# Kernel tuning notes

Measured on AMD Instinct MI355X. Metric: run time of the kernel, lower is better.

The kernel has to match this reference:

```python
import jax, jax.numpy as jnp
import numpy as np

B, N, D, NS, H, ITERS = 64, 4096, 64, 7, 128, 3
EPS = 1e-8
SCALE = D ** -0.5
LN_EPS = 1e-5


def layernorm(x, g, b):
    m = x.mean(-1, keepdims=True)
    v = ((x - m) ** 2).mean(-1, keepdims=True)
    return (x - m) / jnp.sqrt(v + LN_EPS) * g + b


def gru_cell(x, h, W_ih, W_hh, b_ih, b_hh):
    # torch.nn.GRUCell semantics
    gi = x @ W_ih.T + b_ih
    gh = h @ W_hh.T + b_hh
    i_r, i_z, i_n = jnp.split(gi, 3, axis=-1)
    h_r, h_z, h_n = jnp.split(gh, 3, axis=-1)
    r = jax.nn.sigmoid(i_r + h_r)
    z = jax.nn.sigmoid(i_z + h_z)
    n = jnp.tanh(i_n + r * h_n)
    return (1.0 - z) * n + z * h


def setup_inputs() -> dict:
    key = jax.random.key(0)
    ks = jax.random.split(key, 16)
    s = 0.02
    inp = {}
    inp['inputs'] = jax.random.normal(ks[0], (B, N, D), jnp.float32)
    inp['positional_embeddings'] = jax.random.normal(ks[1], (B, N, 4), jnp.float32)
    inp['slots_noise'] = jax.random.normal(ks[2], (B, NS, D), jnp.float32)
    inp['slots_mu'] = jax.random.normal(ks[3], (1, 1, D), jnp.float32)
    inp['slots_sigma'] = jax.random.uniform(ks[4], (1, 1, D), jnp.float32)
    inp['Wq'] = jax.random.normal(ks[5], (D, D), jnp.float32) * s
    inp['bq'] = jnp.zeros((D,), jnp.float32)
    inp['Wk'] = jax.random.normal(ks[6], (D, D), jnp.float32) * s
    inp['bk'] = jnp.zeros((D,), jnp.float32)
    inp['Wv'] = jax.random.normal(ks[7], (D, D), jnp.float32) * s
    inp['bv'] = jnp.zeros((D,), jnp.float32)
    inp['W_ih'] = jax.random.normal(ks[8], (3 * D, D), jnp.float32) * s
    inp['W_hh'] = jax.random.normal(ks[9], (3 * D, D), jnp.float32) * s
    inp['b_ih'] = jnp.zeros((3 * D,), jnp.float32)
    inp['b_hh'] = jnp.zeros((3 * D,), jnp.float32)
    inp['W1'] = jax.random.normal(ks[10], (H, D), jnp.float32) * s
    inp['b1'] = jnp.zeros((H,), jnp.float32)
    inp['W2'] = jax.random.normal(ks[11], (D, H), jnp.float32) * s
    inp['b2'] = jnp.zeros((D,), jnp.float32)
    inp['g_in'] = jnp.ones((D,), jnp.float32)
    inp['be_in'] = jnp.zeros((D,), jnp.float32)
    inp['g_sl'] = jnp.ones((D,), jnp.float32)
    inp['be_sl'] = jnp.zeros((D,), jnp.float32)
    inp['g_ff'] = jnp.ones((D,), jnp.float32)
    inp['be_ff'] = jnp.zeros((D,), jnp.float32)
    return inp


def reference(inputs, positional_embeddings, slots_noise, slots_mu, slots_sigma,
              Wq, bq, Wk, bk, Wv, bv, W_ih, W_hh, b_ih, b_hh,
              W1, b1, W2, b2, g_in, be_in, g_sl, be_sl, g_ff, be_ff):
    b, n, d = inputs.shape
    # slots ~ Normal(mu, sigma), reparameterized with externalized noise
    slots = slots_mu + slots_sigma * slots_noise  # [b, NS, d]
    x = layernorm(inputs, g_in, be_in)
    k = x @ Wk.T + bk  # [b, n, d]
    v = x @ Wv.T + bv  # [b, n, d]
    for _ in range(ITERS):
        slots_prev = slots
        s = layernorm(slots, g_sl, be_sl)
        q = s @ Wq.T + bq  # [b, NS, d]
        dots = jnp.einsum('bid,bjd->bij', q, k) * SCALE  # [b, NS, n]
        attn = jax.nn.softmax(dots, axis=1) + EPS  # softmax over slot axis
        attn = attn / attn.sum(-1, keepdims=True)  # renormalize over inputs
        updates = jnp.einsum('bjd,bij->bid', v, attn)  # [b, NS, d]
        slots = gru_cell(updates.reshape(-1, d), slots_prev.reshape(-1, d),
                         W_ih, W_hh, b_ih, b_hh).reshape(b, -1, d)
        ff = layernorm(slots, g_ff, be_ff)
        slots = slots + (jax.nn.relu(ff @ W1.T + b1) @ W2.T + b2)
    return slots
```

## Files before the change

kernel.cpp:

```cpp
#include <hip/hip_runtime.h>
#include <stdint.h>

#define BB 64
#define NN 4096
#define DD 64
#define NSL 7
#define HH 128
#define NITER 3

typedef __attribute__((ext_vector_type(8))) short short8;
typedef __attribute__((ext_vector_type(4))) float f32x4;

__device__ __forceinline__ unsigned short f2bf(float f){
    union { float f; unsigned int i; } x; x.f = f;
    unsigned int u = x.i;
    u += 0x7fffu + ((u >> 16) & 1u);
    return (unsigned short)(u >> 16);
}
__device__ __forceinline__ unsigned int pack2(float a, float b){
    return (unsigned int)f2bf(a) | ((unsigned int)f2bf(b) << 16);
}
__device__ __forceinline__ short8 f2bf8(float4 a, float4 b){
    short8 r;
    r[0]=(short)f2bf(a.x); r[1]=(short)f2bf(a.y); r[2]=(short)f2bf(a.z); r[3]=(short)f2bf(a.w);
    r[4]=(short)f2bf(b.x); r[5]=(short)f2bf(b.y); r[6]=(short)f2bf(b.z); r[7]=(short)f2bf(b.w);
    return r;
}
__device__ __forceinline__ f32x4 mfma16(short8 a, short8 b, f32x4 c){
    return __builtin_amdgcn_mfma_f32_16x16x32_bf16(a, b, c, 0, 0, 0);
}
__device__ __forceinline__ float sigm(float x){ return 1.f / (1.f + __expf(-x)); }

__global__ __launch_bounds__(256) void ln_kv_kernel(
    const float* __restrict__ inp,
    const float* __restrict__ g_in, const float* __restrict__ be_in,
    const float* __restrict__ Wk, const float* __restrict__ bk,
    const float* __restrict__ Wv, const float* __restrict__ bv,
    unsigned short* __restrict__ k_out, unsigned short* __restrict__ vT_out)
{
    __shared__ __align__(16) unsigned short xn[64 * 72];
    __shared__ __align__(16) unsigned short vt[64 * 72];
    const int t = threadIdx.x;
    const long R0 = (long)blockIdx.x * 64;

    {
        const int m = t >> 2, p = t & 3;
        const float4* rp = reinterpret_cast<const float4*>(inp + (R0 + m) * 64 + p * 16);
        float x[16];
        #pragma unroll
        for (int q4 = 0; q4 < 4; ++q4){
            float4 a = rp[q4];
            x[q4*4+0]=a.x; x[q4*4+1]=a.y; x[q4*4+2]=a.z; x[q4*4+3]=a.w;
        }
        float s = 0.f, ss = 0.f;
        #pragma unroll
        for (int e = 0; e < 16; ++e){ s += x[e]; ss += x[e]*x[e]; }
        s += __shfl_xor(s, 1); ss += __shfl_xor(ss, 1);
        s += __shfl_xor(s, 2); ss += __shfl_xor(ss, 2);
        const float mean = s * 0.015625f;
        const float var  = ss * 0.015625f - mean * mean;
        const float rstd = rsqrtf(var + 1e-5f);
        const float4* gp = reinterpret_cast<const float4*>(g_in + p * 16);
        const float4* bp = reinterpret_cast<const float4*>(be_in + p * 16);
        float gv[16], bev[16];
        #pragma unroll
        for (int q4 = 0; q4 < 4; ++q4){
            float4 a = gp[q4], bb = bp[q4];
            gv[q4*4+0]=a.x; gv[q4*4+1]=a.y; gv[q4*4+2]=a.z; gv[q4*4+3]=a.w;
            bev[q4*4+0]=bb.x; bev[q4*4+1]=bb.y; bev[q4*4+2]=bb.z; bev[q4*4+3]=bb.w;
        }
        unsigned int packed[8];
        #pragma unroll
        for (int e2 = 0; e2 < 8; ++e2){
            float a = (x[e2*2  ] - mean) * rstd * gv[e2*2  ] + bev[e2*2  ];
            float b = (x[e2*2+1] - mean) * rstd * gv[e2*2+1] + bev[e2*2+1];
            packed[e2] = pack2(a, b);
        }
        uint4* xp = reinterpret_cast<uint4*>(xn) + (m * 9 + p * 2);
        xp[0] = make_uint4(packed[0], packed[1], packed[2], packed[3]);
        xp[1] = make_uint4(packed[4], packed[5], packed[6], packed[7]);
    }
    __syncthreads();

    const int lane = t & 63, wave = t >> 6;
    const int n16 = lane & 15, quad = lane >> 4;

    short8 xf0 = *reinterpret_cast<const short8*>(xn + (wave*16 + n16)*72 +      quad*8);
    short8 xf1 = *reinterpret_cast<const short8*>(xn + (wave*16 + n16)*72 + 32 + quad*8);

    f32x4 acck[4];
    #pragma unroll
    for (int mt = 0; mt < 4; ++mt){
        const float* wp = Wk + (mt*16 + n16)*64 + quad*8;
        short8 a0 = f2bf8(*reinterpret_cast<const float4*>(wp),
                          *reinterpret_cast<const float4*>(wp + 4));
        short8 a1 = f2bf8(*reinterpret_cast<const float4*>(wp + 32),
                          *reinterpret_cast<const float4*>(wp + 36));
        f32x4 z = {0.f, 0.f, 0.f, 0.f};
        z = mfma16(a0, xf0, z);
        acck[mt] = mfma16(a1, xf1, z);
    }
    f32x4 accv[4];
    #pragma unroll
    for (int dt = 0; dt < 4; ++dt){
        const float* wp = Wv + (dt*16 + n16)*64 + quad*8;
        short8 b0 = f2bf8(*reinterpret_cast<const float4*>(wp),
                          *reinterpret_cast<const float4*>(wp + 4));
        short8 b1 = f2bf8(*reinterpret_cast<const float4*>(wp + 32),
                          *reinterpret_cast<const float4*>(wp + 36));
        f32x4 z = {0.f, 0.f, 0.f, 0.f};
        z = mfma16(xf0, b0, z);
        accv[dt] = mfma16(xf1, b1, z);
    }
    #pragma unroll
    for (int mt = 0; mt < 4; ++mt){
        const int m0 = mt*16 + quad*4;
        float4 bk4 = *reinterpret_cast<const float4*>(bk + m0);
        uint2 pk;
        pk.x = pack2(acck[mt][0] + bk4.x, acck[mt][1] + bk4.y);
        pk.y = pack2(acck[mt][2] + bk4.z, acck[mt][3] + bk4.w);
        *reinterpret_cast<uint2*>(xn + (wave*16 + n16)*72 + m0) = pk;
    }
    #pragma unroll
    for (int dt = 0; dt < 4; ++dt){
        const int d = dt*16 + n16;
        const float bias = bv[d];
        const int jl = wave*16 + quad*4;
        uint2 pk;
        pk.x = pack2(accv[dt][0] + bias, accv[dt][1] + bias);
        pk.y = pack2(accv[dt][2] + bias, accv[dt][3] + bias);
        *reinterpret_cast<uint2*>(vt + d*72 + jl) = pk;
    }
    __syncthreads();

    {
        const int j = t >> 2, sg = t & 3;
        const uint4* ksrc = reinterpret_cast<const uint4*>(xn + j*72 + sg*16);
        uint4* kdst = reinterpret_cast<uint4*>(k_out + (R0 + j)*64 + sg*16);
        kdst[0] = ksrc[0];
        kdst[1] = ksrc[1];
        const int bidx = (int)(R0 >> 12);
        const int jblk = (int)(R0 & 4095);
        const int d = j;
        const uint4* vsrc = reinterpret_cast<const uint4*>(vt + d*72 + sg*16);
        uint4* vdst = reinterpret_cast<uint4*>(vT_out + ((long)(bidx*64 + d))*4096 + jblk + sg*16);
        vdst[0] = vsrc[0];
        vdst[1] = vsrc[1];
    }
}

__global__ __launch_bounds__(256) void scan_kernel(
    const unsigned short* __restrict__ k_ws, const unsigned short* __restrict__ vT_ws,
    const float* __restrict__ q_ws, float* __restrict__ pu)
{
    __shared__ __align__(16) unsigned short at_all[4][16 * 40];
    __shared__ float red[4][8][80];
    const int t = threadIdx.x, lane = t & 63, wave = t >> 6;
    const int n16 = lane & 15, quad = lane >> 4;
    const int b = blockIdx.x >> 5, seg = blockIdx.x & 31;
    unsigned short* at = at_all[wave];

    for (int idx = lane; idx < 9 * 40; idx += 64){
        int rr = idx / 40, cc = idx - rr * 40;
        at[(7 + rr) * 40 + cc] = (rr == 0 && cc < 32) ? (unsigned short)0x3F80 : (unsigned short)0;
    }

    const int iq = (n16 < NSL) ? n16 : (NSL - 1);
    const float* qp = q_ws + (b*NSL + iq)*64;
    short8 qa0, qa1;
    {
        float4 a0 = *reinterpret_cast<const float4*>(qp + quad*8);
        float4 a1 = *reinterpret_cast<const float4*>(qp + quad*8 + 4);
        float4 b0 = *reinterpret_cast<const float4*>(qp + 32 + quad*8);
        float4 b1 = *reinterpret_cast<const float4*>(qp + 32 + quad*8 + 4);
        qa0 = f2bf8(make_float4(a0.x*0.125f,a0.y*0.125f,a0.z*0.125f,a0.w*0.125f),
                    make_float4(a1.x*0.125f,a1.y*0.125f,a1.z*0.125f,a1.w*0.125f));
        qa1 = f2bf8(make_float4(b0.x*0.125f,b0.y*0.125f,b0.z*0.125f,b0.w*0.125f),
                    make_float4(b1.x*0.125f,b1.y*0.125f,b1.z*0.125f,b1.w*0.125f));
    }

    const int j0 = seg*128 + wave*32;
    const long kbase = (long)b * NN * 64;
    const long vbase = (long)b * 64 * NN;

    #pragma unroll
    for (int tt = 0; tt < 2; ++tt){
        const unsigned short* kp = k_ws + kbase + (long)(j0 + tt*16 + n16)*64 + quad*8;
        short8 kb0 = *reinterpret_cast<const short8*>(kp);
        short8 kb1 = *reinterpret_cast<const short8*>(kp + 32);
        f32x4 dz = {0.f,0.f,0.f,0.f};
        dz = mfma16(qa0, kb0, dz);
        dz = mfma16(qa1, kb1, dz);
        float pm;
        if (quad == 0)      pm = fmaxf(fmaxf(dz[0], dz[1]), fmaxf(dz[2], dz[3]));
        else if (quad == 1) pm = fmaxf(fmaxf(dz[0], dz[1]), dz[2]);
        else                pm = -1e30f;
        pm = fmaxf(pm, __shfl_xor(pm, 16));
        float e0=0.f, e1=0.f, e2=0.f, e3=0.f;
        if (quad == 0){ e0=__expf(dz[0]-pm); e1=__expf(dz[1]-pm); e2=__expf(dz[2]-pm); e3=__expf(dz[3]-pm); }
        else if (quad == 1){ e0=__expf(dz[0]-pm); e1=__expf(dz[1]-pm); e2=__expf(dz[2]-pm); }
        float ps = e0 + e1 + e2 + e3;
        ps += __shfl_xor(ps, 16);
        const float inv = 1.f / ps;
        if (quad == 0){
            at[0*40 + tt*16 + n16] = f2bf(e0*inv);
            at[1*40 + tt*16 + n16] = f2bf(e1*inv);
            at[2*40 + tt*16 + n16] = f2bf(e2*inv);
            at[3*40 + tt*16 + n16] = f2bf(e3*inv);
        } else if (quad == 1){
            at[4*40 + tt*16 + n16] = f2bf(e0*inv);
            at[5*40 + tt*16 + n16] = f2bf(e1*inv);
            at[6*40 + tt*16 + n16] = f2bf(e2*inv);
        }
    }
    __syncthreads();

    short8 aa = *reinterpret_cast<const short8*>(at + n16*40 + quad*8);
    short8 ones;
    { const short ov = (n16 == 0) ? (short)0x3F80 : (short)0;
      #pragma unroll
      for (int z = 0; z < 8; ++z) ones[z] = ov; }

    f32x4 uacc[5];
    #pragma unroll
    for (int t2 = 0; t2 < 4; ++t2){
        const unsigned short* vp = vT_ws + vbase + (long)(t2*16 + n16)*NN + j0 + quad*8;
        short8 vb = *reinterpret_cast<const short8*>(vp);
        f32x4 z = {0.f,0.f,0.f,0.f};
        uacc[t2] = mfma16(aa, vb, z);
    }
    { f32x4 z = {0.f,0.f,0.f,0.f}; uacc[4] = mfma16(aa, ones, z); }

    if (quad < 2){
        #pragma unroll
        for (int r = 0; r < 4; ++r){
            const int i = quad*4 + r;
            #pragma unroll
            for (int t2 = 0; t2 < 5; ++t2)
                red[wave][i][t2*16 + n16] = uacc[t2][r];
        }
    }
    __syncthreads();
    for (int idx = t; idx < 640; idx += 256){
        const int i = idx / 80, cc = idx - i*80;
        float s = red[0][i][cc] + red[1][i][cc] + red[2][i][cc] + red[3][i][cc];
        pu[((long)(b*32 + seg)*8 + i)*80 + cc] = s;
    }
}

__device__ __forceinline__ float dot64(const float* x, const float* w){
    float acc = 0.f;
    const float4* w4 = reinterpret_cast<const float4*>(w);
    #pragma unroll
    for (int e4 = 0; e4 < 16; ++e4){
        float4 wv = w4[e4];
        acc += x[e4*4+0]*wv.x + x[e4*4+1]*wv.y + x[e4*4+2]*wv.z + x[e4*4+3]*wv.w;
    }
    return acc;
}
__device__ __forceinline__ float dot128(const float* x, const float* w){
    float acc = 0.f;
    const float4* w4 = reinterpret_cast<const float4*>(w);
    #pragma unroll
    for (int e4 = 0; e4 < 32; ++e4){
        float4 wv = w4[e4];
        acc += x[e4*4+0]*wv.x + x[e4*4+1]*wv.y + x[e4*4+2]*wv.z + x[e4*4+3]*wv.w;
    }
    return acc;
}

__global__ __launch_bounds__(256) void slot_update_kernel(
    const int mode, const int write_out,
    const float* __restrict__ pu,
    float* __restrict__ slots_ws, float* __restrict__ q_ws,
    const float* __restrict__ noise, const float* __restrict__ mu,
    const float* __restrict__ sigma,
    const float* __restrict__ W_ih, const float* __restrict__ W_hh,
    const float* __restrict__ b_ih, const float* __restrict__ b_hh,
    const float* __restrict__ W1, const float* __restrict__ b1,
    const float* __restrict__ W2, const float* __restrict__ b2,
    const float* __restrict__ g_sl, const float* __restrict__ be_sl,
    const float* __restrict__ g_ff, const float* __restrict__ be_ff,
    const float* __restrict__ Wq, const float* __restrict__ bq,
    float* __restrict__ out)
{
    __shared__ float hprev[64], updv[64], snew[64], ffb[64], h1[128], sfin[64], s2[64];
    __shared__ float redp[4][64], redp7[4][64];
    __shared__ float gi[192], gh[192];
    __shared__ float redA_s;
    const int t = threadIdx.x;
    const int b = blockIdx.x / NSL, i = blockIdx.x % NSL;
    const int lane = t & 63, wave = t >> 6;
    const long rowoff = (long)(b*NSL + i)*64;

    if (mode == 0){
        if (t < 64){
            float v = mu[t] + sigma[t] * noise[rowoff + t];
            sfin[t] = v;
            slots_ws[rowoff + t] = v;
        }
    } else {
        if (t < 64) hprev[t] = slots_ws[rowoff + t];
        {
            const int d = t & 63, g = t >> 6;
            float si = 0.f, s7 = 0.f;
            #pragma unroll
            for (int u = 0; u < 8; ++u){
                const float* base = pu + ((long)(b*32 + g*8 + u)*8)*80;
                si += base[i*80 + d];
                s7 += base[7*80 + d];
            }
            redp[g][d] = si; redp7[g][d] = s7;
        }
        if (wave == 0){
            float a = (lane < 32) ? pu[((long)(b*32 + lane)*8 + i)*80 + 64] : 0.f;
            #pragma unroll
            for (int m = 1; m < 64; m <<= 1) a += __shfl_xor(a, m);
            if (lane == 0) redA_s = a;
        }
        __syncthreads();
        if (t < 64){
            float ri = redp[0][t] + redp[1][t] + redp[2][t] + redp[3][t];
            float r7 = redp7[0][t] + redp7[1][t] + redp7[2][t] + redp7[3][t];
            updv[t] = (ri + 1e-8f * r7) / (redA_s + 4.096e-5f);
        }
        __syncthreads();
        for (int c = t; c < 384; c += 256){
            if (c < 192) gi[c] = b_ih[c] + dot64(updv, W_ih + c*64);
            else { int cc = c - 192; gh[cc] = b_hh[cc] + dot64(hprev, W_hh + cc*64); }
        }
        __syncthreads();
        if (t < 64){
            float rg = sigm(gi[t] + gh[t]);
            float zg = sigm(gi[64+t] + gh[64+t]);
            float ng = tanhf(gi[128+t] + rg * gh[128+t]);
            snew[t] = (1.f - zg) * ng + zg * hprev[t];
        }
        __syncthreads();
        {
            float x = snew[lane];
            float s = x, ss = x * x;
            #pragma unroll
            for (int m = 1; m < 64; m <<= 1){ s += __shfl_xor(s, m); ss += __shfl_xor(ss, m); }
            float mean = s * 0.015625f;
            float var  = ss * 0.015625f - mean * mean;
            float rstd = rsqrtf(var + 1e-5f);
            if (wave == 0) ffb[lane] = (x - mean) * rstd * g_ff[lane] + be_ff[lane];
        }
        __syncthreads();
        if (t < 128){
            float vv = b1[t] + dot64(ffb, W1 + t*64);
            h1[t] = vv > 0.f ? vv : 0.f;
        }
        __syncthreads();
        if (t < 64){
            float o = b2[t] + dot128(h1, W2 + t*128);
            float v = snew[t] + o;
            sfin[t] = v;
            slots_ws[rowoff + t] = v;
            if (write_out) out[rowoff + t] = v;
        }
    }
    __syncthreads();
    {
        float x = sfin[lane];
        float s = x, ss = x * x;
        #pragma unroll
        for (int m = 1; m < 64; m <<= 1){ s += __shfl_xor(s, m); ss += __shfl_xor(ss, m); }
        float mean = s * 0.015625f;
        float var  = ss * 0.015625f - mean * mean;
        float rstd = rsqrtf(var + 1e-5f);
        if (wave == 0) s2[lane] = (x - mean) * rstd * g_sl[lane] + be_sl[lane];
    }
    __syncthreads();
    if (t < 64) q_ws[rowoff + t] = bq[t] + dot64(s2, Wq + t*64);
}

extern "C" void kernel_launch(void* const* d_in, const int* in_sizes, int n_in,
                              void* d_out, int out_size, void* d_ws, size_t ws_size,
                              hipStream_t stream)
{
    const float* inp   = (const float*)d_in[0];
    const float* noise = (const float*)d_in[2];
    const float* mu    = (const float*)d_in[3];
    const float* sigma = (const float*)d_in[4];
    const float* Wq    = (const float*)d_in[5];
    const float* bq    = (const float*)d_in[6];
    const float* Wk    = (const float*)d_in[7];
    const float* bk    = (const float*)d_in[8];
    const float* Wv    = (const float*)d_in[9];
    const float* bv    = (const float*)d_in[10];
    const float* W_ih  = (const float*)d_in[11];
    const float* W_hh  = (const float*)d_in[12];
    const float* b_ih  = (const float*)d_in[13];
    const float* b_hh  = (const float*)d_in[14];
    const float* W1    = (const float*)d_in[15];
    const float* b1    = (const float*)d_in[16];
    const float* W2    = (const float*)d_in[17];
    const float* b2    = (const float*)d_in[18];
    const float* g_in  = (const float*)d_in[19];
    const float* be_in = (const float*)d_in[20];
    const float* g_sl  = (const float*)d_in[21];
    const float* be_sl = (const float*)d_in[22];
    const float* g_ff  = (const float*)d_in[23];
    const float* be_ff = (const float*)d_in[24];
    float* out = (float*)d_out;

    char* w = (char*)d_ws;
    unsigned short* k_ws  = (unsigned short*)(w);
    unsigned short* vT_ws = (unsigned short*)(w + 33554432);
    float* slots_ws       = (float*)(w + 67108864);
    float* q_ws           = (float*)(w + 67108864 + 114688);
    float* pu             = (float*)(w + 67108864 + 229376);

    ln_kv_kernel<<<4096, 256, 0, stream>>>(inp, g_in, be_in, Wk, bk, Wv, bv, k_ws, vT_ws);
    slot_update_kernel<<<448, 256, 0, stream>>>(0, 0, pu, slots_ws, q_ws, noise, mu, sigma,
        W_ih, W_hh, b_ih, b_hh, W1, b1, W2, b2, g_sl, be_sl, g_ff, be_ff, Wq, bq, out);
    for (int it = 0; it < NITER; ++it){
        scan_kernel<<<2048, 256, 0, stream>>>(k_ws, vT_ws, q_ws, pu);
        slot_update_kernel<<<448, 256, 0, stream>>>(1, (it == NITER - 1) ? 1 : 0,
            pu, slots_ws, q_ws, noise, mu, sigma,
            W_ih, W_hh, b_ih, b_hh, W1, b1, W2, b2, g_sl, be_sl, g_ff, be_ff, Wq, bq, out);
    }
}
```

Before: 293.0 us.

## Make LN+KV projection kernel persistent over tiles with register-resident weights

Each block now processes 8 row tiles and converts Wk and Wv to bf16 fragments only once, keeping them in registers. LayerNorm is computed directly in the MFMA operand layout with cross-lane shuffles, so the LDS staging buffers and both __syncthreads are removed. K and transposed V are written straight from the accumulators as 8-byte stores instead of going through LDS and coalesced 16-byte copies. The cost is fewer blocks (512), higher register pressure, and less coalesced global stores, especially for the vT writes, which spread across rows.

Result: faster. 264.9 us (-9.6%).

```diff
diff --git a/kernel.cpp b/kernel.cpp
--- a/kernel.cpp
+++ b/kernel.cpp
@@ -7,6 +7,7 @@
 #define NSL 7
 #define HH 128
 #define NITER 3
+#define TPT 8
 
 typedef __attribute__((ext_vector_type(8))) short short8;
 typedef __attribute__((ext_vector_type(4))) float f32x4;
@@ -38,114 +39,91 @@
     const float* __restrict__ Wv, const float* __restrict__ bv,
     unsigned short* __restrict__ k_out, unsigned short* __restrict__ vT_out)
 {
-    __shared__ __align__(16) unsigned short xn[64 * 72];
-    __shared__ __align__(16) unsigned short vt[64 * 72];
-    const int t = threadIdx.x;
-    const long R0 = (long)blockIdx.x * 64;
-
-    {
-        const int m = t >> 2, p = t & 3;
-        const float4* rp = reinterpret_cast<const float4*>(inp + (R0 + m) * 64 + p * 16);
-        float x[16];
-        #pragma unroll
-        for (int q4 = 0; q4 < 4; ++q4){
-            float4 a = rp[q4];
-            x[q4*4+0]=a.x; x[q4*4+1]=a.y; x[q4*4+2]=a.z; x[q4*4+3]=a.w;
-        }
-        float s = 0.f, ss = 0.f;
-        #pragma unroll
-        for (int e = 0; e < 16; ++e){ s += x[e]; ss += x[e]*x[e]; }
-        s += __shfl_xor(s, 1); ss += __shfl_xor(ss, 1);
-        s += __shfl_xor(s, 2); ss += __shfl_xor(ss, 2);
-        const float mean = s * 0.015625f;
-        const float var  = ss * 0.015625f - mean * mean;
-        const float rstd = rsqrtf(var + 1e-5f);
-        const float4* gp = reinterpret_cast<const float4*>(g_in + p * 16);
-        const float4* bp = reinterpret_cast<const float4*>(be_in + p * 16);
-        float gv[16], bev[16];
-        #pragma unroll
-        for (int q4 = 0; q4 < 4; ++q4){
-            float4 a = gp[q4], bb = bp[q4];
-            gv[q4*4+0]=a.x; gv[q4*4+1]=a.y; gv[q4*4+2]=a.z; gv[q4*4+3]=a.w;
-            bev[q4*4+0]=bb.x; bev[q4*4+1]=bb.y; bev[q4*4+2]=bb.z; bev[q4*4+3]=bb.w;
-        }
-        unsigned int packed[8];
-        #pragma unroll
-        for (int e2 = 0; e2 < 8; ++e2){
-            float a = (x[e2*2  ] - mean) * rstd * gv[e2*2  ] + bev[e2*2  ];
-            float b = (x[e2*2+1] - mean) * rstd * gv[e2*2+1] + bev[e2*2+1];
-            packed[e2] = pack2(a, b);
-        }
-        uint4* xp = reinterpret_cast<uint4*>(xn) + (m * 9 + p * 2);
-        xp[0] = make_uint4(packed[0], packed[1], packed[2], packed[3]);
-        xp[1] = make_uint4(packed[4], packed[5], packed[6], packed[7]);
-    }
-    __syncthreads();
-
-    const int lane = t & 63, wave = t >> 6;
+    const int t = threadIdx.x, lane = t & 63, wave = t >> 6;
     const int n16 = lane & 15, quad = lane >> 4;
 
-    short8 xf0 = *reinterpret_cast<const short8*>(xn + (wave*16 + n16)*72 +      quad*8);
-    short8 xf1 = *reinterpret_cast<const short8*>(xn + (wave*16 + n16)*72 + 32 + quad*8);
-
-    f32x4 acck[4];
+    const float4 gA = *reinterpret_cast<const float4*>(g_in + quad*8);
+    const float4 gB = *reinterpret_cast<const float4*>(g_in + quad*8 + 4);
+    const float4 gC = *reinterpret_cast<const float4*>(g_in + 32 + quad*8);
+    const float4 gD = *reinterpret_cast<const float4*>(g_in + 32 + quad*8 + 4);
+    const float4 eA = *reinterpret_cast<const float4*>(be_in + quad*8);
+    const float4 eB = *reinterpret_cast<const float4*>(be_in + quad*8 + 4);
+    const float4 eC = *reinterpret_cast<const float4*>(be_in + 32 + quad*8);
+    const float4 eD = *reinterpret_cast<const float4*>(be_in + 32 + quad*8 + 4);
+
+    short8 wka0[4], wka1[4], wvb0[4], wvb1[4];
+    float4 bk4[4];
+    float  bvs[4];
     #pragma unroll
     for (int mt = 0; mt < 4; ++mt){
         const float* wp = Wk + (mt*16 + n16)*64 + quad*8;
-        short8 a0 = f2bf8(*reinterpret_cast<const float4*>(wp),
-                          *reinterpret_cast<const float4*>(wp + 4));
-        short8 a1 = f2bf8(*reinterpret_cast<const float4*>(wp + 32),
-                          *reinterpret_cast<const float4*>(wp + 36));
-        f32x4 z = {0.f, 0.f, 0.f, 0.f};
-        z = mfma16(a0, xf0, z);
-        acck[mt] = mfma16(a1, xf1, z);
-    }
-    f32x4 accv[4];
-    #pragma unroll
-    for (int dt = 0; dt < 4; ++dt){
-        const float* wp = Wv + (dt*16 + n16)*64 + quad*8;
-        short8 b0 = f2bf8(*reinterpret_cast<const float4*>(wp),
-                          *reinterpret_cast<const float4*>(wp + 4));
-        short8 b1 = f2bf8(*reinterpret_cast<const float4*>(wp + 32),
-                          *reinterpret_cast<const float4*>(wp + 36));
-        f32x4 z = {0.f, 0.f, 0.f, 0.f};
-        z = mfma16(xf0, b0, z);
-        accv[dt] = mfma16(xf1, b1, z);
-    }
-    #pragma unroll
-    for (int mt = 0; mt < 4; ++mt){
-        const int m0 = mt*16 + quad*4;
-        float4 bk4 = *reinterpret_cast<const float4*>(bk + m0);
-        uint2 pk;
-        pk.x = pack2(acck[mt][0] + bk4.x, acck[mt][1] + bk4.y);
-        pk.y = pack2(acck[mt][2] + bk4.z, acck[mt][3] + bk4.w);
-        *reinterpret_cast<uint2*>(xn + (wave*16 + n16)*72 + m0) = pk;
-    }
-    #pragma unroll
-    for (int dt = 0; dt < 4; ++dt){
-        const int d = dt*16 + n16;
-        const float bias = bv[d];
-        const int jl = wave*16 + quad*4;
-        uint2 pk;
-        pk.x = pack2(accv[dt][0] + bias, accv[dt][1] + bias);
-        pk.y = pack2(accv[dt][2] + bias, accv[dt][3] + bias);
-        *reinterpret_cast<uint2*>(vt + d*72 + jl) = pk;
-    }
-    __syncthreads();
-
-    {
-        const int j = t >> 2, sg = t & 3;
-        const uint4* ksrc = reinterpret_cast<const uint4*>(xn + j*72 + sg*16);
-        uint4* kdst = reinterpret_cast<uint4*>(k_out + (R0 + j)*64 + sg*16);
-        kdst[0] = ksrc[0];
-        kdst[1] = ksrc[1];
-        const int bidx = (int)(R0 >> 12);
-        const int jblk = (int)(R0 & 4095);
-        const int d = j;
-        const uint4* vsrc = reinterpret_cast<const uint4*>(vt + d*72 + sg*16);
-        uint4* vdst = reinterpret_cast<uint4*>(vT_out + ((long)(bidx*64 + d))*4096 + jblk + sg*16);
-        vdst[0] = vsrc[0];
-        vdst[1] = vsrc[1];
+        wka0[mt] = f2bf8(*reinterpret_cast<const float4*>(wp),
+                         *reinterpret_cast<const float4*>(wp + 4));
+        wka1[mt] = f2bf8(*reinterpret_cast<const float4*>(wp + 32),
+                         *reinterpret_cast<const float4*>(wp + 36));
+        const float* vp = Wv + (mt*16 + n16)*64 + quad*8;
+        wvb0[mt] = f2bf8(*reinterpret_cast<const float4*>(vp),
+                         *reinterpret_cast<const float4*>(vp + 4));
+        wvb1[mt] = f2bf8(*reinterpret_cast<const float4*>(vp + 32),
+                         *reinterpret_cast<const float4*>(vp + 36));
+        bk4[mt] = *reinterpret_cast<const float4*>(bk + mt*16 + quad*4);
+        bvs[mt] = bv[mt*16 + n16];
+    }
+
+    for (int c = 0; c < TPT; ++c){
+        const long T0 = ((long)blockIdx.x * TPT + c) * 64;
+        const float* rp = inp + (T0 + wave*16 + n16) * 64;
+        float4 xa = *reinterpret_cast<const float4*>(rp + quad*8);
+        float4 xb = *reinterpret_cast<const float4*>(rp + quad*8 + 4);
+        float4 xc = *reinterpret_cast<const float4*>(rp + 32 + quad*8);
+        float4 xd = *reinterpret_cast<const float4*>(rp + 32 + quad*8 + 4);
+
+        float s  = (xa.x+xa.y+xa.z+xa.w) + (xb.x+xb.y+xb.z+xb.w)
+                 + (xc.x+xc.y+xc.z+xc.w) + (xd.x+xd.y+xd.z+xd.w);
+        float ss = (xa.x*xa.x+xa.y*xa.y+xa.z*xa.z+xa.w*xa.w)
+                 + (xb.x*xb.x+xb.y*xb.y+xb.z*xb.z+xb.w*xb.w)
+                 + (xc.x*xc.x+xc.y*xc.y+xc.z*xc.z+xc.w*xc.w)
+                 + (xd.x*xd.x+xd.y*xd.y+xd.z*xd.z+xd.w*xd.w);
+        s  += __shfl_xor(s, 16);  ss += __shfl_xor(ss, 16);
+        s  += __shfl_xor(s, 32);  ss += __shfl_xor(ss, 32);
+        const float mean = s * 0.015625f;
+        const float rstd = rsqrtf(ss * 0.015625f - mean*mean + 1e-5f);
+
+        float4 ya, yb, yc, yd;
+        ya.x=(xa.x-mean)*rstd*gA.x+eA.x; ya.y=(xa.y-mean)*rstd*gA.y+eA.y;
+        ya.z=(xa.z-mean)*rstd*gA.z+eA.z; ya.w=(xa.w-mean)*rstd*gA.w+eA.w;
+        yb.x=(xb.x-mean)*rstd*gB.x+eB.x; yb.y=(xb.y-mean)*rstd*gB.y+eB.y;
+        yb.z=(xb.z-mean)*rstd*gB.z+eB.z; yb.w=(xb.w-mean)*rstd*gB.w+eB.w;
+        yc.x=(xc.x-mean)*rstd*gC.x+eC.x; yc.y=(xc.y-mean)*rstd*gC.y+eC.y;
+        yc.z=(xc.z-mean)*rstd*gC.z+eC.z; yc.w=(xc.w-mean)*rstd*gC.w+eC.w;
+        yd.x=(xd.x-mean)*rstd*gD.x+eD.x; yd.y=(xd.y-mean)*rstd*gD.y+eD.y;
+        yd.z=(xd.z-mean)*rstd*gD.z+eD.z; yd.w=(xd.w-mean)*rstd*gD.w+eD.w;
+        const short8 xf0 = f2bf8(ya, yb);
+        const short8 xf1 = f2bf8(yc, yd);
+
+        unsigned short* krow = k_out + (T0 + wave*16 + n16)*64;
+        #pragma unroll
+        for (int mt = 0; mt < 4; ++mt){
+            f32x4 z = {0.f,0.f,0.f,0.f};
+            z = mfma16(wka0[mt], xf0, z);
+            z = mfma16(wka1[mt], xf1, z);
+            uint2 pk;
+            pk.x = pack2(z[0]+bk4[mt].x, z[1]+bk4[mt].y);
+            pk.y = pack2(z[2]+bk4[mt].z, z[3]+bk4[mt].w);
+            *reinterpret_cast<uint2*>(krow + mt*16 + quad*4) = pk;
+        }
+        const int bidx = (int)(T0 >> 12);
+        const int jblk = ((int)T0 & 4095) + wave*16 + quad*4;
+        #pragma unroll
+        for (int dt = 0; dt < 4; ++dt){
+            f32x4 z = {0.f,0.f,0.f,0.f};
+            z = mfma16(xf0, wvb0[dt], z);
+            z = mfma16(xf1, wvb1[dt], z);
+            uint2 pk;
+            pk.x = pack2(z[0]+bvs[dt], z[1]+bvs[dt]);
+            pk.y = pack2(z[2]+bvs[dt], z[3]+bvs[dt]);
+            *reinterpret_cast<uint2*>(vT_out + ((long)(bidx*64 + dt*16 + n16))*4096 + jblk) = pk;
+        }
     }
 }
 
@@ -413,7 +391,7 @@
     float* q_ws           = (float*)(w + 67108864 + 114688);
     float* pu             = (float*)(w + 67108864 + 229376);
 
-    ln_kv_kernel<<<4096, 256, 0, stream>>>(inp, g_in, be_in, Wk, bk, Wv, bv, k_ws, vT_ws);
+    ln_kv_kernel<<<4096/TPT, 256, 0, stream>>>(inp, g_in, be_in, Wk, bk, Wv, bv, k_ws, vT_ws);
     slot_update_kernel<<<448, 256, 0, stream>>>(0, 0, pu, slots_ws, q_ws, noise, mu, sigma,
         W_ih, W_hh, b_ih, b_hh, W1, b1, W2, b2, g_sl, be_sl, g_ff, be_ff, Wq, bq, out);
     for (int it = 0; it < NITER; ++it){
```
